# Kernel optimization log

Measured on AMD Instinct MI355X. Metric: run time of the kernel, lower is better.

Reference implementation:

```python
import jax, jax.numpy as jnp
import numpy as np
from jax import lax

B, L = 8, 1024
C_IN, D_MODEL = 3, 512
N_MAMBA, N_TRANS, NHEAD = 2, 2, 8
D_STATE, D_CONV, EXPAND = 16, 4, 2
DI = EXPAND * D_MODEL            # 1024, mamba inner dim
DT_RANK = D_MODEL // 16          # 32
DH = D_MODEL // NHEAD            # 64, head dim
DFF = 4 * D_MODEL


def setup_inputs() -> dict:
    key = jax.random.key(0)
    ks = iter(jax.random.split(key, 64))
    def rn(shape, s=0.05):
        return jax.random.normal(next(ks), shape, jnp.float32) * s
    inp = {
        'x': jax.random.normal(next(ks), (B, C_IN, L), jnp.float32),
        'proj_w': rn((D_MODEL, C_IN)), 'proj_b': rn((D_MODEL,)),
        # stacked per-mamba-layer params (leading dim = N_MAMBA)
        'm_in_w': rn((N_MAMBA, 2 * DI, D_MODEL)),
        'm_conv_w': rn((N_MAMBA, DI, D_CONV)), 'm_conv_b': rn((N_MAMBA, DI)),
        'm_xproj_w': rn((N_MAMBA, DT_RANK + 2 * D_STATE, DI)),
        'm_dt_w': rn((N_MAMBA, DI, DT_RANK)), 'm_dt_b': rn((N_MAMBA, DI)),
        'm_Alog': jnp.tile(jnp.log(jnp.arange(1, D_STATE + 1, dtype=jnp.float32)), (N_MAMBA, DI, 1)),
        'm_D': jnp.ones((N_MAMBA, DI), jnp.float32),
        'm_out_w': rn((N_MAMBA, D_MODEL, DI)),
        'm_ln_w': jnp.ones((N_MAMBA, D_MODEL), jnp.float32), 'm_ln_b': jnp.zeros((N_MAMBA, D_MODEL), jnp.float32),
        # stacked per-transformer-layer params
        't_qkv_w': rn((N_TRANS, 3 * D_MODEL, D_MODEL)), 't_qkv_b': rn((N_TRANS, 3 * D_MODEL)),
        't_ow': rn((N_TRANS, D_MODEL, D_MODEL)), 't_ob': rn((N_TRANS, D_MODEL)),
        't_l1w': rn((N_TRANS, DFF, D_MODEL)), 't_l1b': rn((N_TRANS, DFF)),
        't_l2w': rn((N_TRANS, D_MODEL, DFF)), 't_l2b': rn((N_TRANS, D_MODEL)),
        't_ln1w': jnp.ones((N_TRANS, D_MODEL), jnp.float32), 't_ln1b': jnp.zeros((N_TRANS, D_MODEL), jnp.float32),
        't_ln2w': jnp.ones((N_TRANS, D_MODEL), jnp.float32), 't_ln2b': jnp.zeros((N_TRANS, D_MODEL), jnp.float32),
        'no_w': jnp.ones((D_MODEL,), jnp.float32), 'no_b': jnp.zeros((D_MODEL,), jnp.float32),
    }
    return inp


def _ln(x, w, b, eps=1e-5):
    m = x.mean(-1, keepdims=True)
    v = ((x - m) ** 2).mean(-1, keepdims=True)
    return (x - m) / jnp.sqrt(v + eps) * w + b


def _pos_encoding(length, d):
    pos = jnp.arange(length, dtype=jnp.float32)[:, None]
    div = jnp.exp(jnp.arange(0, d, 2, dtype=jnp.float32) * (-np.log(10000.0) / d))
    pe = jnp.zeros((length, d), jnp.float32)
    pe = pe.at[:, 0::2].set(jnp.sin(pos * div)).at[:, 1::2].set(jnp.cos(pos * div))
    return pe


def _mamba(h, in_w, conv_w, conv_b, xp_w, dt_w, dt_b, Alog, Dp, out_w):
    # h: [B,L,d_model]
    xz = h @ in_w.T                                   # [B,L,2*DI]
    xm, z = jnp.split(xz, 2, axis=-1)
    # causal depthwise conv1d over time
    k = conv_w.T[:, None, :]                          # [D_CONV,1,DI]
    xc = lax.conv_general_dilated(xm, k, (1,), [(D_CONV - 1, 0)],
                                  dimension_numbers=('NWC', 'WIO', 'NWC'),
                                  feature_group_count=DI) + conv_b
    xc = jax.nn.silu(xc)
    xdb = xc @ xp_w.T                                 # [B,L,DT_RANK+2*D_STATE]
    dt = jax.nn.softplus(xdb[..., :DT_RANK] @ dt_w.T + dt_b)   # [B,L,DI]
    Bm = xdb[..., DT_RANK:DT_RANK + D_STATE]          # [B,L,D_STATE]
    Cm = xdb[..., DT_RANK + D_STATE:]                 # [B,L,D_STATE]
    A = -jnp.exp(Alog)                                # [DI,D_STATE]

    def step(state, t):
        dt_t, B_t, C_t, x_t = t                       # [B,DI],[B,S],[B,S],[B,DI]
        dA = jnp.exp(dt_t[..., None] * A)             # [B,DI,S]
        state = state * dA + (dt_t * x_t)[..., None] * B_t[:, None, :]
        y = jnp.einsum('bds,bs->bd', state, C_t)
        return state, y

    init = jnp.zeros((h.shape[0], DI, D_STATE), h.dtype)
    seq = (dt.transpose(1, 0, 2), Bm.transpose(1, 0, 2), Cm.transpose(1, 0, 2), xc.transpose(1, 0, 2))
    _, ys = lax.scan(step, init, seq)                 # ys: [L,B,DI]
    y = ys.transpose(1, 0, 2) + Dp * xc
    y = y * jax.nn.silu(z)
    return y @ out_w.T                                # [B,L,d_model]


def _transformer_layer(h, qkv_w, qkv_b, ow, ob, l1w, l1b, l2w, l2b, ln1w, ln1b, ln2w, ln2b):
    Bt, Lt, d = h.shape
    qkv = h @ qkv_w.T + qkv_b
    q, k, v = jnp.split(qkv, 3, axis=-1)
    q = q.reshape(Bt, Lt, NHEAD, DH); k = k.reshape(Bt, Lt, NHEAD, DH); v = v.reshape(Bt, Lt, NHEAD, DH)
    sc = jnp.einsum('blhd,bmhd->bhlm', q, k) / np.sqrt(DH).astype(np.float32)
    a = jax.nn.softmax(sc, axis=-1)
    o = jnp.einsum('bhlm,bmhd->blhd', a, v).reshape(Bt, Lt, d)
    h = _ln(h + o @ ow.T + ob, ln1w, ln1b)
    ff = jax.nn.relu(h @ l1w.T + l1b) @ l2w.T + l2b
    return _ln(h + ff, ln2w, ln2b)


def reference(x, proj_w, proj_b, m_in_w, m_conv_w, m_conv_b, m_xproj_w, m_dt_w, m_dt_b,
              m_Alog, m_D, m_out_w, m_ln_w, m_ln_b, t_qkv_w, t_qkv_b, t_ow, t_ob,
              t_l1w, t_l1b, t_l2w, t_l2b, t_ln1w, t_ln1b, t_ln2w, t_ln2b, no_w, no_b):
    # proj_in: 1x1 conv == pointwise linear over channels; output [B,L,d]
    h = jnp.einsum('bcl,dc->bld', x, proj_w) + proj_b
    for i in range(N_MAMBA):
        h = _ln(h + _mamba(h, m_in_w[i], m_conv_w[i], m_conv_b[i], m_xproj_w[i],
                           m_dt_w[i], m_dt_b[i], m_Alog[i], m_D[i], m_out_w[i]),
                m_ln_w[i], m_ln_b[i])
    h = h + _pos_encoding(h.shape[1], D_MODEL)
    for i in range(N_TRANS):
        h = _transformer_layer(h, t_qkv_w[i], t_qkv_b[i], t_ow[i], t_ob[i],
                               t_l1w[i], t_l1b[i], t_l2w[i], t_l2b[i],
                               t_ln1w[i], t_ln1b[i], t_ln2w[i], t_ln2b[i])
    h = _ln(h, no_w, no_b)
    return h, h.mean(axis=1)
```

## Files before the change

kernel.cpp:

```cpp
#include <hip/hip_runtime.h>
#include <cstddef>

#define BATCH 8
#define LSEQ 1024
#define DMODEL 512
#define DINNER 1024
#define DSTATE 16
#define DTRANK 32
#define NHEAD 8
#define DHEAD 64
#define DFF 2048
#define MTOK 8192
#define NCHUNK 16
#define CLEN 64

typedef __attribute__((ext_vector_type(8))) short bfrag;
typedef __attribute__((ext_vector_type(4))) float f32x4;
typedef __attribute__((ext_vector_type(4))) unsigned short us4;
typedef unsigned short ushort_t;

__device__ __forceinline__ float silu_f(float x) { return x / (1.f + __expf(-x)); }

__device__ __forceinline__ unsigned short f2bf(float f) {
  unsigned u = __float_as_uint(f);
  return (unsigned short)((u + 0x7FFFu + ((u >> 16) & 1u)) >> 16);
}

__device__ __forceinline__ void gll16(const ushort_t* g, ushort_t* l) {
  __builtin_amdgcn_global_load_lds(
      (const __attribute__((address_space(1))) unsigned int*)g,
      (__attribute__((address_space(3))) unsigned int*)l, 16, 0, 0);
}

__global__ __launch_bounds__(256) void cvt_bf16(const float* __restrict__ s,
                                                ushort_t* __restrict__ d, int n4) {
  int i = blockIdx.x * 256 + threadIdx.x;
  if (i >= n4) return;
  float4 v = ((const float4*)s)[i];
  us4 o = {f2bf(v.x), f2bf(v.y), f2bf(v.z), f2bf(v.w)};
  ((us4*)d)[i] = o;
}

__global__ __launch_bounds__(256) void proj_kernel(const float* __restrict__ x,
                                                   const float* __restrict__ pw,
                                                   const float* __restrict__ pb,
                                                   float* __restrict__ h,
                                                   ushort_t* __restrict__ hbf) {
  int idx = blockIdx.x * 256 + threadIdx.x;
  int d = idx & 511;
  int l = (idx >> 9) & 1023;
  int b = idx >> 19;
  const float* xb = x + (size_t)b * 3 * 1024 + l;
  float v = pb[d] + xb[0] * pw[d * 3] + xb[1024] * pw[d * 3 + 1] + xb[2048] * pw[d * 3 + 2];
  h[idx] = v;
  hbf[idx] = f2bf(v);
}

template <int ACT, int CBF, int SPLITK>
__global__ __launch_bounds__(256) void gemm_gll(const ushort_t* __restrict__ A,
                                                const ushort_t* __restrict__ W,
                                                const float* __restrict__ bias,
                                                void* __restrict__ Cp,
                                                int K, int lda, int ldc) {
  __shared__ ushort_t sA[2][4096];
  __shared__ ushort_t sB[2][4096];
  const int bm = blockIdx.y * 128, bn = blockIdx.x * 128;
  const int tid = threadIdx.x;
  const int wid = tid >> 6, lane = tid & 63;
  const int wr = wid >> 1, wc = wid & 1;
  const int lr = lane & 15, ls = lane >> 4;
  const int sw = ls ^ ((lr >> 1) & 3);

  const int kseg = K / SPLITK;
  const int kbeg = (SPLITK > 1) ? blockIdx.z * kseg : 0;

  const int c0 = wid * 128 + lane;
  const int c1 = c0 + 64;
  const int r0 = c0 >> 2, s0 = (c0 & 3) ^ ((r0 >> 1) & 3);
  const int r1 = c1 >> 2, s1 = (c1 & 3) ^ ((r1 >> 1) & 3);
  const ushort_t* gA0 = A + (size_t)(bm + r0) * lda + kbeg + s0 * 8;
  const ushort_t* gA1 = A + (size_t)(bm + r1) * lda + kbeg + s1 * 8;
  const ushort_t* gB0 = W + (size_t)(bn + r0) * K + kbeg + s0 * 8;
  const ushort_t* gB1 = W + (size_t)(bn + r1) * K + kbeg + s1 * 8;

  f32x4 acc[4][4];
#pragma unroll
  for (int i = 0; i < 4; ++i)
#pragma unroll
    for (int j = 0; j < 4; ++j) acc[i][j] = (f32x4)(0.f);

#define STAGE(buf, step)                                           \
  do {                                                             \
    gll16(gA0 + (step) * 32, &sA[buf][wid * 1024]);                \
    gll16(gA1 + (step) * 32, &sA[buf][wid * 1024 + 512]);          \
    gll16(gB0 + (step) * 32, &sB[buf][wid * 1024]);                \
    gll16(gB1 + (step) * 32, &sB[buf][wid * 1024 + 512]);          \
  } while (0)

  const int NT = kseg / 32;
  STAGE(0, 0);
  for (int t = 0; t < NT; ++t) {
    const int cur = t & 1;
    if (t + 1 < NT) {
      STAGE(cur ^ 1, t + 1);
      asm volatile("s_waitcnt vmcnt(4)" ::: "memory");
    } else {
      asm volatile("s_waitcnt vmcnt(0)" ::: "memory");
    }
    __builtin_amdgcn_sched_barrier(0);
    __builtin_amdgcn_s_barrier();
    __builtin_amdgcn_sched_barrier(0);

    bfrag af[4], bf[4];
#pragma unroll
    for (int mi = 0; mi < 4; ++mi) {
      int row = wr * 64 + mi * 16 + lr;
      af[mi] = *(const bfrag*)&sA[cur][(size_t)((row << 2) + sw) * 8];
    }
#pragma unroll
    for (int nj = 0; nj < 4; ++nj) {
      int col = wc * 64 + nj * 16 + lr;
      bf[nj] = *(const bfrag*)&sB[cur][(size_t)((col << 2) + sw) * 8];
    }
#pragma unroll
    for (int mi = 0; mi < 4; ++mi)
#pragma unroll
      for (int nj = 0; nj < 4; ++nj)
        acc[mi][nj] = __builtin_amdgcn_mfma_f32_16x16x32_bf16(af[mi], bf[nj], acc[mi][nj], 0, 0, 0);

    __builtin_amdgcn_s_barrier();
    __builtin_amdgcn_sched_barrier(0);
  }
#undef STAGE

  if (SPLITK > 1) {
    float* Cz = (float*)Cp + (size_t)blockIdx.z * 8192 * ldc;
#pragma unroll
    for (int nj = 0; nj < 4; ++nj) {
      int col = bn + wc * 64 + nj * 16 + lr;
#pragma unroll
      for (int mi = 0; mi < 4; ++mi) {
        int row0 = bm + wr * 64 + mi * 16 + ls * 4;
#pragma unroll
        for (int r = 0; r < 4; ++r)
          Cz[(size_t)(row0 + r) * ldc + col] = acc[mi][nj][r];
      }
    }
  } else {
#pragma unroll
    for (int nj = 0; nj < 4; ++nj) {
      int col = bn + wc * 64 + nj * 16 + lr;
      float bv = bias ? bias[col] : 0.f;
#pragma unroll
      for (int mi = 0; mi < 4; ++mi) {
        int row0 = bm + wr * 64 + mi * 16 + ls * 4;
#pragma unroll
        for (int r = 0; r < 4; ++r) {
          float v = acc[mi][nj][r] + bv;
          if (ACT == 1) v = fmaxf(v, 0.f);
          if (CBF)
            ((ushort_t*)Cp)[(size_t)(row0 + r) * ldc + col] = f2bf(v);
          else
            ((float*)Cp)[(size_t)(row0 + r) * ldc + col] = v;
        }
      }
    }
  }
}

__global__ __launch_bounds__(256) void splitk_reduce(const float* __restrict__ p,
                                                     const float* __restrict__ bias,
                                                     float* __restrict__ out) {
  int i = blockIdx.x * 256 + threadIdx.x;
  float4 a = ((const float4*)p)[i];
  float4 b = ((const float4*)p)[i + 1048576];
  float4 o = {a.x + b.x, a.y + b.y, a.z + b.z, a.w + b.w};
  if (bias) {
    float4 bb = ((const float4*)bias)[i & 127];
    o.x += bb.x; o.y += bb.y; o.z += bb.z; o.w += bb.w;
  }
  ((float4*)out)[i] = o;
}

template <int ACT>
__global__ __launch_bounds__(256) void gemm_tn(const float* __restrict__ A,
                                               const float* __restrict__ W,
                                               const float* __restrict__ bias,
                                               float* __restrict__ C,
                                               int M, int N, int K, int lda, int ldc) {
  __shared__ float As[16][65];
  __shared__ float Ws[16][65];
  const int bm = blockIdx.y * 64, bn = blockIdx.x * 64;
  const int tid = threadIdx.x;
  const int lk = tid & 15, lr = tid >> 4;
  const int tx = tid & 15, ty = tid >> 4;
  float acc[4][4] = {};
  for (int k0 = 0; k0 < K; k0 += 16) {
#pragma unroll
    for (int i = 0; i < 4; ++i) {
      As[lk][lr + 16 * i] = A[(size_t)(bm + lr + 16 * i) * lda + k0 + lk];
      Ws[lk][lr + 16 * i] = W[(size_t)(bn + lr + 16 * i) * K + k0 + lk];
    }
    __syncthreads();
#pragma unroll
    for (int kk = 0; kk < 16; ++kk) {
      float a[4], w[4];
#pragma unroll
      for (int i = 0; i < 4; ++i) a[i] = As[kk][ty + 16 * i];
#pragma unroll
      for (int j = 0; j < 4; ++j) w[j] = Ws[kk][tx + 16 * j];
#pragma unroll
      for (int i = 0; i < 4; ++i)
#pragma unroll
        for (int j = 0; j < 4; ++j) acc[i][j] += a[i] * w[j];
    }
    __syncthreads();
  }
#pragma unroll
  for (int i = 0; i < 4; ++i) {
    int r = bm + ty + 16 * i;
#pragma unroll
    for (int j = 0; j < 4; ++j) {
      int c = bn + tx + 16 * j;
      float v = acc[i][j];
      if (bias) v += bias[c];
      if (ACT == 2) v = (v > 20.f) ? v : log1pf(__expf(v));
      C[(size_t)r * ldc + c] = v;
    }
  }
}

__global__ __launch_bounds__(256) void conv_silu_kernel(const float* __restrict__ xz,
                                                        const float* __restrict__ cw,
                                                        const float* __restrict__ cb,
                                                        float* __restrict__ xc) {
  int idx = blockIdx.x * 256 + threadIdx.x;
  int d = idx & 1023;
  int t = (idx >> 10) & 1023;
  int b = idx >> 20;
  float acc = cb[d];
#pragma unroll
  for (int w = 0; w < 4; ++w) {
    int tt = t - 3 + w;
    if (tt >= 0) acc += xz[(((size_t)(b * 1024 + tt)) << 11) + d] * cw[d * 4 + w];
  }
  xc[idx] = silu_f(acc);
}

__global__ __launch_bounds__(256) void scan_pass1(const float* __restrict__ dt,
                                                  const float* __restrict__ xdb,
                                                  const float* __restrict__ xc,
                                                  const float* __restrict__ Alog,
                                                  float* __restrict__ scrP,
                                                  float* __restrict__ scrL) {
  int idx = blockIdx.x * 256 + threadIdx.x;
  int sh = idx & 3;
  int d = (idx >> 2) & 1023;
  int c = (idx >> 12) & 15;
  int b = idx >> 16;
  float A[4], st[4], P[4];
#pragma unroll
  for (int s = 0; s < 4; ++s) {
    A[s] = -__expf(Alog[d * 16 + sh * 4 + s]);
    st[s] = 0.f;
    P[s] = 1.f;
  }
  int t0 = c * CLEN;
  size_t base = (((size_t)(b * 1024 + t0)) << 10) + d;
  const float* xb = xdb + (size_t)(b * 1024 + t0) * 64 + 32 + sh * 4;
  float dtv = dt[base], xv = xc[base];
  for (int t = 0; t < CLEN; ++t) {
    float dtn = 0.f, xvn = 0.f;
    if (t + 1 < CLEN) { dtn = dt[base + 1024]; xvn = xc[base + 1024]; }
    float4 Bv = *(const float4*)xb;
    float dx = dtv * xv;
    float e0 = __expf(dtv * A[0]), e1 = __expf(dtv * A[1]);
    float e2 = __expf(dtv * A[2]), e3 = __expf(dtv * A[3]);
    st[0] = st[0] * e0 + dx * Bv.x; P[0] *= e0;
    st[1] = st[1] * e1 + dx * Bv.y; P[1] *= e1;
    st[2] = st[2] * e2 + dx * Bv.z; P[2] *= e2;
    st[3] = st[3] * e3 + dx * Bv.w; P[3] *= e3;
    base += 1024; xb += 64;
    dtv = dtn; xv = xvn;
  }
  size_t pbase = (((size_t)((b * 16 + c) * 16 + sh * 4)) << 10) + d;
#pragma unroll
  for (int s = 0; s < 4; ++s) {
    scrP[pbase + ((size_t)s << 10)] = P[s];
    scrL[pbase + ((size_t)s << 10)] = st[s];
  }
}

__global__ __launch_bounds__(256) void scan_pass2(const float* __restrict__ scrP,
                                                  float* __restrict__ scrL) {
  int idx = blockIdx.x * 256 + threadIdx.x;
  int d = idx & 1023;
  int s = (idx >> 10) & 15;
  int b = idx >> 14;
  float cur = 0.f;
  for (int c = 0; c < 16; ++c) {
    size_t o = (((size_t)(((b * 16 + c) * 16) + s)) << 10) + d;
    float P = scrP[o];
    float loc = scrL[o];
    scrL[o] = cur;
    cur = cur * P + loc;
  }
}

__global__ __launch_bounds__(256) void scan_pass3(const float* __restrict__ dt,
                                                  const float* __restrict__ xdb,
                                                  const float* __restrict__ xc,
                                                  const float* __restrict__ xz,
                                                  ushort_t* __restrict__ ybf,
                                                  const float* __restrict__ Alog,
                                                  const float* __restrict__ Dp,
                                                  const float* __restrict__ scrL) {
  int idx = blockIdx.x * 256 + threadIdx.x;
  int sh = idx & 3;
  int d = (idx >> 2) & 1023;
  int c = (idx >> 12) & 15;
  int b = idx >> 16;
  float A[4], st[4];
  size_t pbase = (((size_t)((b * 16 + c) * 16 + sh * 4)) << 10) + d;
#pragma unroll
  for (int s = 0; s < 4; ++s) {
    A[s] = -__expf(Alog[d * 16 + sh * 4 + s]);
    st[s] = scrL[pbase + ((size_t)s << 10)];
  }
  float Dv = Dp[d];
  int t0 = c * CLEN;
  size_t base = (((size_t)(b * 1024 + t0)) << 10) + d;
  size_t zoff = ((((size_t)(b * 1024 + t0)) << 11)) + 1024 + d;
  const float* xb = xdb + (size_t)(b * 1024 + t0) * 64 + 32 + sh * 4;
  float dtv = dt[base], xv = xc[base], zv = xz[zoff];
  for (int t = 0; t < CLEN; ++t) {
    float dtn = 0.f, xvn = 0.f, zvn = 0.f;
    if (t + 1 < CLEN) {
      dtn = dt[base + 1024]; xvn = xc[base + 1024]; zvn = xz[zoff + 2048];
    }
    float4 Bv = *(const float4*)xb;
    float4 Cv = *(const float4*)(xb + 16);
    float dx = dtv * xv;
    float e0 = __expf(dtv * A[0]), e1 = __expf(dtv * A[1]);
    float e2 = __expf(dtv * A[2]), e3 = __expf(dtv * A[3]);
    st[0] = st[0] * e0 + dx * Bv.x;
    st[1] = st[1] * e1 + dx * Bv.y;
    st[2] = st[2] * e2 + dx * Bv.z;
    st[3] = st[3] * e3 + dx * Bv.w;
    float acc = st[0] * Cv.x + st[1] * Cv.y + st[2] * Cv.z + st[3] * Cv.w;
    acc += __shfl_xor(acc, 1);
    acc += __shfl_xor(acc, 2);
    if (sh == 0)
      ybf[base] = f2bf((acc + Dv * xv) * silu_f(zv));
    base += 1024; zoff += 2048; xb += 64;
    dtv = dtn; xv = xvn; zv = zvn;
  }
}

__global__ __launch_bounds__(128) void resid_ln_kernel(const float* __restrict__ x,
                                                       const float* __restrict__ add,
                                                       const float* __restrict__ w,
                                                       const float* __restrict__ bias,
                                                       float* __restrict__ out,
                                                       ushort_t* __restrict__ out_bf) {
  int row = blockIdx.x, tid = threadIdx.x;
  float4 v = ((const float4*)(x + (size_t)row * 512))[tid];
  if (add) {
    float4 a = ((const float4*)(add + (size_t)row * 512))[tid];
    v.x += a.x; v.y += a.y; v.z += a.z; v.w += a.w;
  }
  float s = v.x + v.y + v.z + v.w;
  float ss = v.x * v.x + v.y * v.y + v.z * v.z + v.w * v.w;
#pragma unroll
  for (int o = 32; o; o >>= 1) {
    s += __shfl_xor(s, o);
    ss += __shfl_xor(ss, o);
  }
  __shared__ float red[4];
  int wid = tid >> 6;
  if ((tid & 63) == 0) { red[wid] = s; red[2 + wid] = ss; }
  __syncthreads();
  s = red[0] + red[1];
  ss = red[2] + red[3];
  float mean = s * (1.f / 512.f);
  float var = ss * (1.f / 512.f) - mean * mean;
  float inv = rsqrtf(var + 1e-5f);
  float4 wv = ((const float4*)w)[tid];
  float4 bv = ((const float4*)bias)[tid];
  float4 ov;
  ov.x = (v.x - mean) * inv * wv.x + bv.x;
  ov.y = (v.y - mean) * inv * wv.y + bv.y;
  ov.z = (v.z - mean) * inv * wv.z + bv.z;
  ov.w = (v.w - mean) * inv * wv.w + bv.w;
  ((float4*)(out + (size_t)row * 512))[tid] = ov;
  if (out_bf) {
    us4 ob = {f2bf(ov.x), f2bf(ov.y), f2bf(ov.z), f2bf(ov.w)};
    ((us4*)(out_bf + (size_t)row * 512))[tid] = ob;
  }
}

__global__ __launch_bounds__(256) void posenc_kernel(float* __restrict__ h,
                                                     ushort_t* __restrict__ hbf) {
  int idx = blockIdx.x * 256 + threadIdx.x;
  int d = idx & 511;
  int l = (idx >> 9) & 1023;
  float freq = __expf(-(float)(d & ~1) * (9.210340371976184f / 512.f));
  float ang = (float)l * freq;
  float v = h[idx] + ((d & 1) ? cosf(ang) : sinf(ang));
  h[idx] = v;
  hbf[idx] = f2bf(v);
}

__global__ __launch_bounds__(256) void attn_mfma(const ushort_t* __restrict__ qkv,
                                                 ushort_t* __restrict__ ao) {
  __shared__ unsigned short Qs[4096];
  __shared__ unsigned short Ks[4096];
  __shared__ unsigned short Vt[4096];
  __shared__ unsigned short Ps[4096];
  const int tid = threadIdx.x;
  const int blk = blockIdx.x;
  const int qt = blk & 15, hh = (blk >> 4) & 7, b = blk >> 7;
  const int l0 = qt * 64;
  const size_t bb = (size_t)b * 1024 * 1536;

  const int srow = tid >> 2;
  const int sdb = (tid & 3) << 4;
  const int sc0 = sdb >> 3;

  {
    const ushort_t* qp = qkv + bb + (size_t)(l0 + srow) * 1536 + hh * 64 + sdb;
    *(bfrag*)&Qs[srow * 64 + ((sc0 ^ (srow & 7)) << 3)] = *(const bfrag*)qp;
    *(bfrag*)&Qs[srow * 64 + (((sc0 + 1) ^ (srow & 7)) << 3)] = *(const bfrag*)(qp + 8);
  }

  const int wid = tid >> 6, lane = tid & 63;
  const int l15 = lane & 15, rg = lane >> 4;
  const int l7 = l15 & 7;
  float m[4], lsum[4];
  f32x4 oacc[4];
#pragma unroll
  for (int r = 0; r < 4; ++r) { m[r] = -1e30f; lsum[r] = 0.f; }
#pragma unroll
  for (int nt = 0; nt < 4; ++nt) oacc[nt] = (f32x4)(0.f);

  for (int jt = 0; jt < 16; ++jt) {
    {
      const ushort_t* kp = qkv + bb + (size_t)(jt * 64 + srow) * 1536 + hh * 64 + 512 + sdb;
      *(bfrag*)&Ks[srow * 64 + ((sc0 ^ (srow & 7)) << 3)] = *(const bfrag*)kp;
      *(bfrag*)&Ks[srow * 64 + (((sc0 + 1) ^ (srow & 7)) << 3)] = *(const bfrag*)(kp + 8);
      const ushort_t* vp = kp + 512;
      unsigned short vv[16];
      *(bfrag*)&vv[0] = *(const bfrag*)vp;
      *(bfrag*)&vv[8] = *(const bfrag*)(vp + 8);
#pragma unroll
      for (int j = 0; j < 16; ++j) {
        int dd = sdb + j;
        Vt[dd * 64 + (((srow >> 3) ^ (dd & 7)) << 3) + (srow & 7)] = vv[j];
      }
    }
    __syncthreads();

    bfrag aq[2];
#pragma unroll
    for (int ks = 0; ks < 2; ++ks)
      aq[ks] = *(const bfrag*)&Qs[(wid * 16 + l15) * 64 + (((ks * 4 + rg) ^ l7) << 3)];
    f32x4 sc[4];
#pragma unroll
    for (int nt = 0; nt < 4; ++nt) {
      f32x4 s = (f32x4)(0.f);
#pragma unroll
      for (int ks = 0; ks < 2; ++ks) {
        bfrag bk = *(const bfrag*)&Ks[(nt * 16 + l15) * 64 + (((ks * 4 + rg) ^ l7) << 3)];
        s = __builtin_amdgcn_mfma_f32_16x16x32_bf16(aq[ks], bk, s, 0, 0, 0);
      }
      sc[nt] = s * 0.125f;
    }

#pragma unroll
    for (int r = 0; r < 4; ++r) {
      float mc = fmaxf(fmaxf(sc[0][r], sc[1][r]), fmaxf(sc[2][r], sc[3][r]));
#pragma unroll
      for (int o = 8; o; o >>= 1) mc = fmaxf(mc, __shfl_xor(mc, o));
      float mn = fmaxf(m[r], mc);
      float al = __expf(m[r] - mn);
      m[r] = mn;
      int prow = rg * 4 + r;
      float ps = 0.f;
#pragma unroll
      for (int nt = 0; nt < 4; ++nt) {
        float p = __expf(sc[nt][r] - mn);
        ps += p;
        int col = nt * 16 + l15;
        Ps[wid * 1024 + prow * 64 + ((((col >> 3) ^ (prow & 7))) << 3) + (col & 7)] = f2bf(p);
      }
#pragma unroll
      for (int o = 8; o; o >>= 1) ps += __shfl_xor(ps, o);
      lsum[r] = lsum[r] * al + ps;
#pragma unroll
      for (int nt = 0; nt < 4; ++nt) oacc[nt][r] *= al;
    }

    bfrag ap[2];
#pragma unroll
    for (int ks = 0; ks < 2; ++ks)
      ap[ks] = *(const bfrag*)&Ps[wid * 1024 + l15 * 64 + (((ks * 4 + rg) ^ l7) << 3)];
#pragma unroll
    for (int nt = 0; nt < 4; ++nt) {
#pragma unroll
      for (int ks = 0; ks < 2; ++ks) {
        bfrag bv = *(const bfrag*)&Vt[(nt * 16 + l15) * 64 + (((ks * 4 + rg) ^ l7) << 3)];
        oacc[nt] = __builtin_amdgcn_mfma_f32_16x16x32_bf16(ap[ks], bv, oacc[nt], 0, 0, 0);
      }
    }
    __syncthreads();
  }

#pragma unroll
  for (int r = 0; r < 4; ++r) {
    float inv = 1.f / lsum[r];
    int row = l0 + wid * 16 + rg * 4 + r;
    ushort_t* op = ao + ((size_t)(b * 1024 + row)) * 512 + hh * 64;
#pragma unroll
    for (int nt = 0; nt < 4; ++nt) op[nt * 16 + l15] = f2bf(oacc[nt][r] * inv);
  }
}

__global__ __launch_bounds__(512) void mean_part(const float* __restrict__ h,
                                                 float* __restrict__ part) {
  int blk = blockIdx.x;
  int b = blk >> 4, lc = blk & 15, d = threadIdx.x;
  float s = 0.f;
  int l0 = lc * 64;
  for (int l = l0; l < l0 + 64; ++l) s += h[(((size_t)(b * 1024 + l)) << 9) + d];
  part[((size_t)blk << 9) + d] = s;
}
__global__ __launch_bounds__(256) void mean_final(const float* __restrict__ part,
                                                  float* __restrict__ out2) {
  int i = blockIdx.x * 256 + threadIdx.x;
  int b = i >> 9, d = i & 511;
  float s = 0.f;
#pragma unroll
  for (int c = 0; c < 16; ++c) s += part[(((size_t)(b * 16 + c)) << 9) + d];
  out2[i] = s * (1.f / 1024.f);
}

extern "C" void kernel_launch(void* const* d_in, const int* in_sizes, int n_in,
                              void* d_out, int out_size, void* d_ws, size_t ws_size,
                              hipStream_t stream) {
  const float* x        = (const float*)d_in[0];
  const float* proj_w   = (const float*)d_in[1];
  const float* proj_b   = (const float*)d_in[2];
  const float* m_in_w   = (const float*)d_in[3];
  const float* m_conv_w = (const float*)d_in[4];
  const float* m_conv_b = (const float*)d_in[5];
  const float* m_xproj_w= (const float*)d_in[6];
  const float* m_dt_w   = (const float*)d_in[7];
  const float* m_dt_b   = (const float*)d_in[8];
  const float* m_Alog   = (const float*)d_in[9];
  const float* m_D      = (const float*)d_in[10];
  const float* m_out_w  = (const float*)d_in[11];
  const float* m_ln_w   = (const float*)d_in[12];
  const float* m_ln_b   = (const float*)d_in[13];
  const float* t_qkv_w  = (const float*)d_in[14];
  const float* t_qkv_b  = (const float*)d_in[15];
  const float* t_ow     = (const float*)d_in[16];
  const float* t_ob     = (const float*)d_in[17];
  const float* t_l1w    = (const float*)d_in[18];
  const float* t_l1b    = (const float*)d_in[19];
  const float* t_l2w    = (const float*)d_in[20];
  const float* t_l2b    = (const float*)d_in[21];
  const float* t_ln1w   = (const float*)d_in[22];
  const float* t_ln1b   = (const float*)d_in[23];
  const float* t_ln2w   = (const float*)d_in[24];
  const float* t_ln2b   = (const float*)d_in[25];
  const float* no_w     = (const float*)d_in[26];
  const float* no_b     = (const float*)d_in[27];

  float* ws   = (float*)d_ws;
  float* h    = ws;
  ushort_t* h_bf = (ushort_t*)(ws + 4194304);
  float* bufA = ws + 6291456;
  float* bufB = bufA + 16777216;
  float* bufC = bufB + 8388608;
  float* bufE = bufC + 8388608;
  float* bufF = bufE + 4194304;
  ushort_t* y_bf = (ushort_t*)(bufF + 524288);
  ushort_t* wbf  = (ushort_t*)(bufF + 524288 + 4194304);
  float* scrP = bufE;
  float* scrL = bufE + 2097152;
  const int M = MTOK;

  ushort_t* wIN  = wbf;
  ushort_t* wOUT = wbf + 2097152;
  ushort_t* wQKV = wbf + 3145728;
  ushort_t* wOW  = wbf + 4718592;
  ushort_t* wL1  = wbf + 5242880;
  ushort_t* wL2  = wbf + 7340032;

  cvt_bf16<<<2048, 256, 0, stream>>>(m_in_w,  wIN,  524288);
  cvt_bf16<<<1024, 256, 0, stream>>>(m_out_w, wOUT, 262144);
  cvt_bf16<<<1536, 256, 0, stream>>>(t_qkv_w, wQKV, 393216);
  cvt_bf16<<< 512, 256, 0, stream>>>(t_ow,    wOW,  131072);
  cvt_bf16<<<2048, 256, 0, stream>>>(t_l1w,   wL1,  524288);
  cvt_bf16<<<2048, 256, 0, stream>>>(t_l2w,   wL2,  524288);

  proj_kernel<<<16384, 256, 0, stream>>>(x, proj_w, proj_b, h, h_bf);

  for (int i = 0; i < 2; ++i) {
    gemm_gll<0, 0, 1><<<dim3(16, 64), 256, 0, stream>>>(
        h_bf, wIN + (size_t)i * 1048576, nullptr, bufA, DMODEL, DMODEL, 2 * DINNER);
    conv_silu_kernel<<<32768, 256, 0, stream>>>(bufA, m_conv_w + i * DINNER * 4,
                                                m_conv_b + i * DINNER, bufB);
    gemm_tn<0><<<dim3(1, M / 64), 256, 0, stream>>>(
        bufB, m_xproj_w + (size_t)i * 64 * DINNER, nullptr, bufF,
        M, 64, DINNER, DINNER, 64);
    gemm_tn<2><<<dim3(DINNER / 64, M / 64), 256, 0, stream>>>(
        bufF, m_dt_w + (size_t)i * DINNER * DTRANK, m_dt_b + i * DINNER, bufC,
        M, DINNER, DTRANK, 64, DINNER);
    scan_pass1<<<2048, 256, 0, stream>>>(bufC, bufF, bufB,
                                         m_Alog + (size_t)i * DINNER * DSTATE, scrP, scrL);
    scan_pass2<<<512, 256, 0, stream>>>(scrP, scrL);
    scan_pass3<<<2048, 256, 0, stream>>>(bufC, bufF, bufB, bufA, y_bf,
                                         m_Alog + (size_t)i * DINNER * DSTATE,
                                         m_D + i * DINNER, scrL);
    gemm_gll<0, 0, 2><<<dim3(4, 64, 2), 256, 0, stream>>>(
        y_bf, wOUT + (size_t)i * 524288, nullptr, bufC, DINNER, DINNER, DMODEL);
    splitk_reduce<<<4096, 256, 0, stream>>>(bufC, nullptr, bufE);
    resid_ln_kernel<<<8192, 128, 0, stream>>>(h, bufE, m_ln_w + i * DMODEL,
                                              m_ln_b + i * DMODEL, h, h_bf);
  }

  posenc_kernel<<<16384, 256, 0, stream>>>(h, h_bf);

  for (int i = 0; i < 2; ++i) {
    gemm_gll<0, 1, 1><<<dim3(12, 64), 256, 0, stream>>>(
        h_bf, wQKV + (size_t)i * 786432, t_qkv_b + i * 3 * DMODEL, bufA,
        DMODEL, DMODEL, 3 * DMODEL);
    attn_mfma<<<1024, 256, 0, stream>>>((const ushort_t*)bufA, (ushort_t*)bufB);
    gemm_gll<0, 0, 2><<<dim3(4, 64, 2), 256, 0, stream>>>(
        (const ushort_t*)bufB, wOW + (size_t)i * 262144, nullptr, bufC,
        DMODEL, DMODEL, DMODEL);
    splitk_reduce<<<4096, 256, 0, stream>>>(bufC, t_ob + i * DMODEL, bufE);
    resid_ln_kernel<<<8192, 128, 0, stream>>>(h, bufE, t_ln1w + i * DMODEL,
                                              t_ln1b + i * DMODEL, h, h_bf);
    gemm_gll<1, 1, 1><<<dim3(16, 64), 256, 0, stream>>>(
        h_bf, wL1 + (size_t)i * 1048576, t_l1b + i * DFF, bufA,
        DMODEL, DMODEL, DFF);
    gemm_gll<0, 0, 2><<<dim3(4, 64, 2), 256, 0, stream>>>(
        (const ushort_t*)bufA, wL2 + (size_t)i * 1048576, nullptr, bufC,
        DFF, DFF, DMODEL);
    splitk_reduce<<<4096, 256, 0, stream>>>(bufC, t_l2b + i * DMODEL, bufE);
    resid_ln_kernel<<<8192, 128, 0, stream>>>(h, bufE, t_ln2w + i * DMODEL,
                                              t_ln2b + i * DMODEL, h, h_bf);
  }

  float* out_h = (float*)d_out;
  resid_ln_kernel<<<8192, 128, 0, stream>>>(h, nullptr, no_w, no_b, out_h, nullptr);
  mean_part<<<128, 512, 0, stream>>>(out_h, bufF);
  mean_final<<<16, 256, 0, stream>>>(bufF, out_h + 4194304);
}
```

Measured before the change: 1.145 ms.

## Move Mamba x_proj and dt_proj GEMMs to bf16 MFMA with split-K

```diff
diff --git a/kernel.cpp b/kernel.cpp
--- a/kernel.cpp
+++ b/kernel.cpp
@@ -24,6 +24,9 @@
 __device__ __forceinline__ unsigned short f2bf(float f) {
   unsigned u = __float_as_uint(f);
   return (unsigned short)((u + 0x7FFFu + ((u >> 16) & 1u)) >> 16);
+}
+__device__ __forceinline__ float bf2f(ushort_t u) {
+  return __uint_as_float((unsigned)u << 16);
 }
 
 __device__ __forceinline__ void gll16(const ushort_t* g, ushort_t* l) {
@@ -56,18 +59,20 @@
   hbf[idx] = f2bf(v);
 }
 
-template <int ACT, int CBF, int SPLITK>
+template <int ACT, int CBF, int SPLITK, int BN>
 __global__ __launch_bounds__(256) void gemm_gll(const ushort_t* __restrict__ A,
                                                 const ushort_t* __restrict__ W,
                                                 const float* __restrict__ bias,
                                                 void* __restrict__ Cp,
                                                 int K, int lda, int ldc) {
   __shared__ ushort_t sA[2][4096];
-  __shared__ ushort_t sB[2][4096];
-  const int bm = blockIdx.y * 128, bn = blockIdx.x * 128;
+  __shared__ ushort_t sB[2][BN * 32];
+  constexpr int MREP = (BN == 128) ? 4 : 2;
+  const int bm = blockIdx.y * 128, bn = blockIdx.x * BN;
   const int tid = threadIdx.x;
   const int wid = tid >> 6, lane = tid & 63;
-  const int wr = wid >> 1, wc = wid & 1;
+  const int wrb = (BN == 128) ? (wid >> 1) * 64 : wid * 32;
+  const int wcb = (BN == 128) ? (wid & 1) * 64 : 0;
   const int lr = lane & 15, ls = lane >> 4;
   const int sw = ls ^ ((lr >> 1) & 3);
 
@@ -80,21 +85,33 @@
   const int r1 = c1 >> 2, s1 = (c1 & 3) ^ ((r1 >> 1) & 3);
   const ushort_t* gA0 = A + (size_t)(bm + r0) * lda + kbeg + s0 * 8;
   const ushort_t* gA1 = A + (size_t)(bm + r1) * lda + kbeg + s1 * 8;
-  const ushort_t* gB0 = W + (size_t)(bn + r0) * K + kbeg + s0 * 8;
-  const ushort_t* gB1 = W + (size_t)(bn + r1) * K + kbeg + s1 * 8;
-
-  f32x4 acc[4][4];
-#pragma unroll
-  for (int i = 0; i < 4; ++i)
+  const ushort_t* gB0;
+  const ushort_t* gB1 = nullptr;
+  if constexpr (BN == 128) {
+    gB0 = W + (size_t)(bn + r0) * K + kbeg + s0 * 8;
+    gB1 = W + (size_t)(bn + r1) * K + kbeg + s1 * 8;
+  } else {
+    const int cb = wid * 64 + lane;
+    const int rb = cb >> 2, sb2 = (cb & 3) ^ ((rb >> 1) & 3);
+    gB0 = W + (size_t)(bn + rb) * K + kbeg + sb2 * 8;
+  }
+
+  f32x4 acc[MREP][4];
+#pragma unroll
+  for (int i = 0; i < MREP; ++i)
 #pragma unroll
     for (int j = 0; j < 4; ++j) acc[i][j] = (f32x4)(0.f);
 
-#define STAGE(buf, step)                                           \
-  do {                                                             \
-    gll16(gA0 + (step) * 32, &sA[buf][wid * 1024]);                \
-    gll16(gA1 + (step) * 32, &sA[buf][wid * 1024 + 512]);          \
-    gll16(gB0 + (step) * 32, &sB[buf][wid * 1024]);                \
-    gll16(gB1 + (step) * 32, &sB[buf][wid * 1024 + 512]);          \
+#define STAGE(buf, step)                                             \
+  do {                                                               \
+    gll16(gA0 + (step) * 32, &sA[buf][wid * 1024]);                  \
+    gll16(gA1 + (step) * 32, &sA[buf][wid * 1024 + 512]);            \
+    if constexpr (BN == 128) {                                       \
+      gll16(gB0 + (step) * 32, &sB[buf][wid * 1024]);                \
+      gll16(gB1 + (step) * 32, &sB[buf][wid * 1024 + 512]);          \
+    } else {                                                         \
+      gll16(gB0 + (step) * 32, &sB[buf][wid * 512]);                 \
+    }                                                                \
   } while (0)
 
   const int NT = kseg / 32;
@@ -103,7 +120,10 @@
     const int cur = t & 1;
     if (t + 1 < NT) {
       STAGE(cur ^ 1, t + 1);
-      asm volatile("s_waitcnt vmcnt(4)" ::: "memory");
+      if constexpr (BN == 128)
+        asm volatile("s_waitcnt vmcnt(4)" ::: "memory");
+      else
+        asm volatile("s_waitcnt vmcnt(3)" ::: "memory");
     } else {
       asm volatile("s_waitcnt vmcnt(0)" ::: "memory");
     }
@@ -111,19 +131,19 @@
     __builtin_amdgcn_s_barrier();
     __builtin_amdgcn_sched_barrier(0);
 
-    bfrag af[4], bf[4];
-#pragma unroll
-    for (int mi = 0; mi < 4; ++mi) {
-      int row = wr * 64 + mi * 16 + lr;
+    bfrag af[MREP], bf[4];
+#pragma unroll
+    for (int mi = 0; mi < MREP; ++mi) {
+      int row = wrb + mi * 16 + lr;
       af[mi] = *(const bfrag*)&sA[cur][(size_t)((row << 2) + sw) * 8];
     }
 #pragma unroll
     for (int nj = 0; nj < 4; ++nj) {
-      int col = wc * 64 + nj * 16 + lr;
+      int col = wcb + nj * 16 + lr;
       bf[nj] = *(const bfrag*)&sB[cur][(size_t)((col << 2) + sw) * 8];
     }
 #pragma unroll
-    for (int mi = 0; mi < 4; ++mi)
+    for (int mi = 0; mi < MREP; ++mi)
 #pragma unroll
       for (int nj = 0; nj < 4; ++nj)
         acc[mi][nj] = __builtin_amdgcn_mfma_f32_16x16x32_bf16(af[mi], bf[nj], acc[mi][nj], 0, 0, 0);
@@ -137,10 +157,10 @@
     float* Cz = (float*)Cp + (size_t)blockIdx.z * 8192 * ldc;
 #pragma unroll
     for (int nj = 0; nj < 4; ++nj) {
-      int col = bn + wc * 64 + nj * 16 + lr;
-#pragma unroll
-      for (int mi = 0; mi < 4; ++mi) {
-        int row0 = bm + wr * 64 + mi * 16 + ls * 4;
+      int col = bn + wcb + nj * 16 + lr;
+#pragma unroll
+      for (int mi = 0; mi < MREP; ++mi) {
+        int row0 = bm + wrb + mi * 16 + ls * 4;
 #pragma unroll
         for (int r = 0; r < 4; ++r)
           Cz[(size_t)(row0 + r) * ldc + col] = acc[mi][nj][r];
@@ -149,15 +169,16 @@
   } else {
 #pragma unroll
     for (int nj = 0; nj < 4; ++nj) {
-      int col = bn + wc * 64 + nj * 16 + lr;
+      int col = bn + wcb + nj * 16 + lr;
       float bv = bias ? bias[col] : 0.f;
 #pragma unroll
-      for (int mi = 0; mi < 4; ++mi) {
-        int row0 = bm + wr * 64 + mi * 16 + ls * 4;
+      for (int mi = 0; mi < MREP; ++mi) {
+        int row0 = bm + wrb + mi * 16 + ls * 4;
 #pragma unroll
         for (int r = 0; r < 4; ++r) {
           float v = acc[mi][nj][r] + bv;
           if (ACT == 1) v = fmaxf(v, 0.f);
+          if (ACT == 2) v = (v > 20.f) ? v : log1pf(__expf(v));
           if (CBF)
             ((ushort_t*)Cp)[(size_t)(row0 + r) * ldc + col] = f2bf(v);
           else
@@ -182,58 +203,25 @@
   ((float4*)out)[i] = o;
 }
 
-template <int ACT>
-__global__ __launch_bounds__(256) void gemm_tn(const float* __restrict__ A,
-                                               const float* __restrict__ W,
-                                               const float* __restrict__ bias,
-                                               float* __restrict__ C,
-                                               int M, int N, int K, int lda, int ldc) {
-  __shared__ float As[16][65];
-  __shared__ float Ws[16][65];
-  const int bm = blockIdx.y * 64, bn = blockIdx.x * 64;
-  const int tid = threadIdx.x;
-  const int lk = tid & 15, lr = tid >> 4;
-  const int tx = tid & 15, ty = tid >> 4;
-  float acc[4][4] = {};
-  for (int k0 = 0; k0 < K; k0 += 16) {
-#pragma unroll
-    for (int i = 0; i < 4; ++i) {
-      As[lk][lr + 16 * i] = A[(size_t)(bm + lr + 16 * i) * lda + k0 + lk];
-      Ws[lk][lr + 16 * i] = W[(size_t)(bn + lr + 16 * i) * K + k0 + lk];
-    }
-    __syncthreads();
-#pragma unroll
-    for (int kk = 0; kk < 16; ++kk) {
-      float a[4], w[4];
-#pragma unroll
-      for (int i = 0; i < 4; ++i) a[i] = As[kk][ty + 16 * i];
-#pragma unroll
-      for (int j = 0; j < 4; ++j) w[j] = Ws[kk][tx + 16 * j];
-#pragma unroll
-      for (int i = 0; i < 4; ++i)
-#pragma unroll
-        for (int j = 0; j < 4; ++j) acc[i][j] += a[i] * w[j];
-    }
-    __syncthreads();
-  }
-#pragma unroll
-  for (int i = 0; i < 4; ++i) {
-    int r = bm + ty + 16 * i;
-#pragma unroll
-    for (int j = 0; j < 4; ++j) {
-      int c = bn + tx + 16 * j;
-      float v = acc[i][j];
-      if (bias) v += bias[c];
-      if (ACT == 2) v = (v > 20.f) ? v : log1pf(__expf(v));
-      C[(size_t)r * ldc + c] = v;
-    }
-  }
+__global__ __launch_bounds__(256) void reduce8_xdb(const float* __restrict__ p,
+                                                   float* __restrict__ xdb,
+                                                   ushort_t* __restrict__ xdb_bf) {
+  int i = blockIdx.x * 256 + threadIdx.x;
+  float4 a = ((const float4*)p)[i];
+#pragma unroll
+  for (int z = 1; z < 8; ++z) {
+    float4 b = ((const float4*)p)[i + z * 131072];
+    a.x += b.x; a.y += b.y; a.z += b.z; a.w += b.w;
+  }
+  ((float4*)xdb)[i] = a;
+  us4 o = {f2bf(a.x), f2bf(a.y), f2bf(a.z), f2bf(a.w)};
+  ((us4*)xdb_bf)[i] = o;
 }
 
 __global__ __launch_bounds__(256) void conv_silu_kernel(const float* __restrict__ xz,
                                                         const float* __restrict__ cw,
                                                         const float* __restrict__ cb,
-                                                        float* __restrict__ xc) {
+                                                        ushort_t* __restrict__ xc) {
   int idx = blockIdx.x * 256 + threadIdx.x;
   int d = idx & 1023;
   int t = (idx >> 10) & 1023;
@@ -244,12 +232,12 @@
     int tt = t - 3 + w;
     if (tt >= 0) acc += xz[(((size_t)(b * 1024 + tt)) << 11) + d] * cw[d * 4 + w];
   }
-  xc[idx] = silu_f(acc);
+  xc[idx] = f2bf(silu_f(acc));
 }
 
 __global__ __launch_bounds__(256) void scan_pass1(const float* __restrict__ dt,
                                                   const float* __restrict__ xdb,
-                                                  const float* __restrict__ xc,
+                                                  const ushort_t* __restrict__ xc,
                                                   const float* __restrict__ Alog,
                                                   float* __restrict__ scrP,
                                                   float* __restrict__ scrL) {
@@ -268,10 +256,10 @@
   int t0 = c * CLEN;
   size_t base = (((size_t)(b * 1024 + t0)) << 10) + d;
   const float* xb = xdb + (size_t)(b * 1024 + t0) * 64 + 32 + sh * 4;
-  float dtv = dt[base], xv = xc[base];
+  float dtv = dt[base], xv = bf2f(xc[base]);
   for (int t = 0; t < CLEN; ++t) {
     float dtn = 0.f, xvn = 0.f;
-    if (t + 1 < CLEN) { dtn = dt[base + 1024]; xvn = xc[base + 1024]; }
+    if (t + 1 < CLEN) { dtn = dt[base + 1024]; xvn = bf2f(xc[base + 1024]); }
     float4 Bv = *(const float4*)xb;
     float dx = dtv * xv;
     float e0 = __expf(dtv * A[0]), e1 = __expf(dtv * A[1]);
@@ -309,7 +297,7 @@
 
 __global__ __launch_bounds__(256) void scan_pass3(const float* __restrict__ dt,
                                                   const float* __restrict__ xdb,
-                                                  const float* __restrict__ xc,
+                                                  const ushort_t* __restrict__ xc,
                                                   const float* __restrict__ xz,
                                                   ushort_t* __restrict__ ybf,
                                                   const float* __restrict__ Alog,
@@ -332,11 +320,11 @@
   size_t base = (((size_t)(b * 1024 + t0)) << 10) + d;
   size_t zoff = ((((size_t)(b * 1024 + t0)) << 11)) + 1024 + d;
   const float* xb = xdb + (size_t)(b * 1024 + t0) * 64 + 32 + sh * 4;
-  float dtv = dt[base], xv = xc[base], zv = xz[zoff];
+  float dtv = dt[base], xv = bf2f(xc[base]), zv = xz[zoff];
   for (int t = 0; t < CLEN; ++t) {
     float dtn = 0.f, xvn = 0.f, zvn = 0.f;
     if (t + 1 < CLEN) {
-      dtn = dt[base + 1024]; xvn = xc[base + 1024]; zvn = xz[zoff + 2048];
+      dtn = dt[base + 1024]; xvn = bf2f(xc[base + 1024]); zvn = xz[zoff + 2048];
     }
     float4 Bv = *(const float4*)xb;
     float4 Cv = *(const float4*)(xb + 16);
@@ -588,7 +576,6 @@
   ushort_t* wbf  = (ushort_t*)(bufF + 524288 + 4194304);
   float* scrP = bufE;
   float* scrL = bufE + 2097152;
-  const int M = MTOK;
 
   ushort_t* wIN  = wbf;
   ushort_t* wOUT = wbf + 2097152;
@@ -596,6 +583,9 @@
   ushort_t* wOW  = wbf + 4718592;
   ushort_t* wL1  = wbf + 5242880;
   ushort_t* wL2  = wbf + 7340032;
+  ushort_t* wXP  = wbf + 9437184;
+  ushort_t* wDT  = wbf + 9568256;
+  ushort_t* xdb_bf = wbf + 9633792;
 
   cvt_bf16<<<2048, 256, 0, stream>>>(m_in_w,  wIN,  524288);
   cvt_bf16<<<1024, 256, 0, stream>>>(m_out_w, wOUT, 262144);
@@ -603,27 +593,30 @@
   cvt_bf16<<< 512, 256, 0, stream>>>(t_ow,    wOW,  131072);
   cvt_bf16<<<2048, 256, 0, stream>>>(t_l1w,   wL1,  524288);
   cvt_bf16<<<2048, 256, 0, stream>>>(t_l2w,   wL2,  524288);
+  cvt_bf16<<< 128, 256, 0, stream>>>(m_xproj_w, wXP, 32768);
+  cvt_bf16<<<  64, 256, 0, stream>>>(m_dt_w,  wDT,  16384);
 
   proj_kernel<<<16384, 256, 0, stream>>>(x, proj_w, proj_b, h, h_bf);
 
   for (int i = 0; i < 2; ++i) {
-    gemm_gll<0, 0, 1><<<dim3(16, 64), 256, 0, stream>>>(
+    gemm_gll<0, 0, 1, 128><<<dim3(16, 64), 256, 0, stream>>>(
         h_bf, wIN + (size_t)i * 1048576, nullptr, bufA, DMODEL, DMODEL, 2 * DINNER);
     conv_silu_kernel<<<32768, 256, 0, stream>>>(bufA, m_conv_w + i * DINNER * 4,
-                                                m_conv_b + i * DINNER, bufB);
-    gemm_tn<0><<<dim3(1, M / 64), 256, 0, stream>>>(
-        bufB, m_xproj_w + (size_t)i * 64 * DINNER, nullptr, bufF,
-        M, 64, DINNER, DINNER, 64);
-    gemm_tn<2><<<dim3(DINNER / 64, M / 64), 256, 0, stream>>>(
-        bufF, m_dt_w + (size_t)i * DINNER * DTRANK, m_dt_b + i * DINNER, bufC,
-        M, DINNER, DTRANK, 64, DINNER);
-    scan_pass1<<<2048, 256, 0, stream>>>(bufC, bufF, bufB,
+                                                m_conv_b + i * DINNER, (ushort_t*)bufB);
+    gemm_gll<0, 0, 8, 64><<<dim3(1, 64, 8), 256, 0, stream>>>(
+        (const ushort_t*)bufB, wXP + (size_t)i * 65536, nullptr, bufC,
+        DINNER, DINNER, 64);
+    reduce8_xdb<<<512, 256, 0, stream>>>(bufC, bufF, xdb_bf);
+    gemm_gll<2, 0, 1, 128><<<dim3(8, 64), 256, 0, stream>>>(
+        xdb_bf, wDT + (size_t)i * 32768, m_dt_b + i * DINNER, bufC,
+        DTRANK, 64, DINNER);
+    scan_pass1<<<2048, 256, 0, stream>>>(bufC, bufF, (const ushort_t*)bufB,
                                          m_Alog + (size_t)i * DINNER * DSTATE, scrP, scrL);
     scan_pass2<<<512, 256, 0, stream>>>(scrP, scrL);
-    scan_pass3<<<2048, 256, 0, stream>>>(bufC, bufF, bufB, bufA, y_bf,
+    scan_pass3<<<2048, 256, 0, stream>>>(bufC, bufF, (const ushort_t*)bufB, bufA, y_bf,
                                          m_Alog + (size_t)i * DINNER * DSTATE,
                                          m_D + i * DINNER, scrL);
-    gemm_gll<0, 0, 2><<<dim3(4, 64, 2), 256, 0, stream>>>(
+    gemm_gll<0, 0, 2, 128><<<dim3(4, 64, 2), 256, 0, stream>>>(
         y_bf, wOUT + (size_t)i * 524288, nullptr, bufC, DINNER, DINNER, DMODEL);
     splitk_reduce<<<4096, 256, 0, stream>>>(bufC, nullptr, bufE);
     resid_ln_kernel<<<8192, 128, 0, stream>>>(h, bufE, m_ln_w + i * DMODEL,
@@ -633,20 +626,20 @@
   posenc_kernel<<<16384, 256, 0, stream>>>(h, h_bf);
 
   for (int i = 0; i < 2; ++i) {
-    gemm_gll<0, 1, 1><<<dim3(12, 64), 256, 0, stream>>>(
+    gemm_gll<0, 1, 1, 128><<<dim3(12, 64), 256, 0, stream>>>(
         h_bf, wQKV + (size_t)i * 786432, t_qkv_b + i * 3 * DMODEL, bufA,
         DMODEL, DMODEL, 3 * DMODEL);
     attn_mfma<<<1024, 256, 0, stream>>>((const ushort_t*)bufA, (ushort_t*)bufB);
-    gemm_gll<0, 0, 2><<<dim3(4, 64, 2), 256, 0, stream>>>(
+    gemm_gll<0, 0, 2, 128><<<dim3(4, 64, 2), 256, 0, stream>>>(
         (const ushort_t*)bufB, wOW + (size_t)i * 262144, nullptr, bufC,
         DMODEL, DMODEL, DMODEL);
     splitk_reduce<<<4096, 256, 0, stream>>>(bufC, t_ob + i * DMODEL, bufE);
     resid_ln_kernel<<<8192, 128, 0, stream>>>(h, bufE, t_ln1w + i * DMODEL,
                                               t_ln1b + i * DMODEL, h, h_bf);
-    gemm_gll<1, 1, 1><<<dim3(16, 64), 256, 0, stream>>>(
+    gemm_gll<1, 1, 1, 128><<<dim3(16, 64), 256, 0, stream>>>(
         h_bf, wL1 + (size_t)i * 1048576, t_l1b + i * DFF, bufA,
         DMODEL, DMODEL, DFF);
-    gemm_gll<0, 0, 2><<<dim3(4, 64, 2), 256, 0, stream>>>(
+    gemm_gll<0, 0, 2, 128><<<dim3(4, 64, 2), 256, 0, stream>>>(
         (const ushort_t*)bufA, wL2 + (size_t)i * 1048576, nullptr, bufC,
         DFF, DFF, DMODEL);
     splitk_reduce<<<4096, 256, 0, stream>>>(bufC, t_l2b + i * DMODEL, bufE);
```

Result: faster. 987.4 us (-13.7%).
